# Kernel optimization log

Measured on AMD Instinct MI355X. Metric: run time of the kernel, lower is better.

The kernel has to match this reference:

```python
import jax, jax.numpy as jnp
import numpy as np

BONE_NUM = 16
THRESH = 0.7


def masked_l2(out, tar, mask):
    # out, tar: [B, C, H, W]; mask: [B, H, W]
    diff_norm = jnp.linalg.norm(out - tar, axis=1)          # [B, H, W]
    masked = jnp.where(mask > THRESH, diff_norm, 0.0)
    B = out.shape[0]
    flat_m = masked.reshape(B, -1)
    flat_d = diff_norm.reshape(B, -1)
    cnt = jnp.sum(flat_m != 0, axis=1)                       # device-side nonzero count
    per_sample = jnp.where(
        cnt > 0,
        flat_m.sum(axis=1) / jnp.maximum(cnt, 1).astype(flat_m.dtype),
        flat_d.mean(axis=1),
    )
    return per_sample.mean()


def pose_nocs_loss(pred_joint_map, pred_joint_score, out_mask, tar_joints):
    # pred_joint_map: [B, bn*3, H, W]; pred_joint_score: [B, bn, H, W]
    # out_mask: [B, H, W]; tar_joints: [B, bn, 3]
    B, _, H, W = pred_joint_map.shape
    bn = BONE_NUM
    jm = pred_joint_map.reshape(B, bn, 3, H, W) * out_mask[:, None, None]
    score = jax.nn.sigmoid(pred_joint_score) * out_mask[:, None]        # [B, bn, H, W]
    denom = score.reshape(B, bn, -1).sum(axis=2)[:, :, None, None] + 1e-5
    score_map = score / denom
    jm = jax.lax.stop_gradient(jm) * score_map[:, :, None]              # [B, bn, 3, H, W]
    pred_joint = jm.reshape(B, bn, 3, -1).sum(axis=3)                   # [B, bn, 3]
    loss = jnp.linalg.norm(pred_joint - tar_joints, axis=2).sum()
    return loss / (B * bn)


def setup_inputs() -> dict:
    key = jax.random.key(0)
    k1, k2, k3 = jax.random.split(key, 3)
    B, H, W = 4, 256, 256
    bn = BONE_NUM
    output = jax.random.normal(k1, (B, 4 + bn * 8 + 2, H, W), dtype=jnp.float32)
    tar_maps = jax.random.uniform(k2, (B, 4 + bn * 6 + 1, H, W), dtype=jnp.float32)
    tar_pose = jax.random.normal(k3, (B, bn, 6), dtype=jnp.float32)
    return {"output": output, "tar_maps": tar_maps, "tar_pose": tar_pose}


def reference(output, tar_maps, tar_pose):
    bn = BONE_NUM
    B = output.shape[0]

    # --- slice predictions ---
    pred_nocs = output[:, 0:3]
    mask_logits = output[:, 3]                                # sigmoid applied below
    pred_loc_map = jax.nn.sigmoid(output[:, 4:4 + bn * 3])
    pred_rot_map = jax.nn.sigmoid(output[:, 4 + bn * 3:4 + bn * 6])
    pred_skin_seg = output[:, 4 + bn * 6:4 + bn * 7 + 2]       # [B, bn+2, H, W]
    pred_joint_score = output[:, 4 + bn * 7 + 2:4 + bn * 8 + 2]  # [B, bn, H, W]

    # --- slice targets ---
    target_nocs = tar_maps[:, 0:3]
    target_mask = tar_maps[:, 3]
    tar_loc_map = jax.nn.sigmoid(tar_maps[:, 4:4 + bn * 3])
    tar_rot_map = jax.nn.sigmoid(tar_maps[:, 4 + bn * 3:4 + bn * 6])
    tar_skin_seg = tar_maps[:, 4 + bn * 6].astype(jnp.int32)   # [B, H, W]
    tar_loc = jax.nn.sigmoid(tar_pose[:, :, 0:3])
    tar_rot = jax.nn.sigmoid(tar_pose[:, :, 3:6])

    # --- BCE mask loss (on sigmoid(mask_logits) vs target_mask), stable form ---
    mask_loss = -jnp.mean(
        target_mask * jax.nn.log_sigmoid(mask_logits)
        + (1.0 - target_mask) * jax.nn.log_sigmoid(-mask_logits)
    )

    # --- masked L2 losses ---
    nocs_loss = masked_l2(pred_nocs, target_nocs, target_mask)
    loc_map_loss = masked_l2(pred_loc_map, tar_loc_map, target_mask)
    rot_map_loss = masked_l2(pred_rot_map, tar_rot_map, target_mask)

    # --- skinning cross entropy ---
    logits = jnp.transpose(pred_skin_seg, (0, 2, 3, 1)).reshape(-1, bn + 2)
    labels = tar_skin_seg.reshape(-1)
    logp = jax.nn.log_softmax(logits, axis=-1)
    skin_loss = -jnp.mean(jnp.take_along_axis(logp, labels[:, None], axis=1))

    # --- pose losses ---
    loc_loss = pose_nocs_loss(pred_loc_map, pred_joint_score, target_mask, tar_loc)
    rot_loss = pose_nocs_loss(pred_rot_map, pred_joint_score, target_mask, tar_rot)

    return jnp.stack([nocs_loss, mask_loss, loc_loss, loc_map_loss,
                      rot_loss, rot_map_loss, skin_loss])
```

## Files before the change

### kernel.cpp

```cpp
#include <hip/hip_runtime.h>
#include <math.h>

#define HW 65536
#define BN 16


__device__ __forceinline__ float fsig(float x) {
    return __builtin_amdgcn_rcpf(1.0f + __expf(-x));
}
__device__ __forceinline__ float sq(float x) { return x * x; }

__device__ __forceinline__ float wred(float v) {
#pragma unroll
    for (int off = 32; off; off >>= 1) v += __shfl_xor(v, off, 64);
    return v;
}

__global__ __launch_bounds__(256) void mvpm_pix2(const float* __restrict__ outp,
                                                 const float* __restrict__ tarp,
                                                 float* __restrict__ ws) {
    const int b = blockIdx.y;
    const int t = blockIdx.x * 256 + threadIdx.x;
    const int C2 = HW / 2;
    const float2* ob = (const float2*)(outp + (size_t)b * 134 * HW) + t;
    const float2* tb = (const float2*)(tarp + (size_t)b * 101 * HW) + t;
    const int lane = threadIdx.x & 63;
    const int wv = threadIdx.x >> 6;

    const float2 m2 = tb[3 * C2];
    const float2 ml = ob[3 * C2];
    const float2 a0 = ob[0], a1 = ob[C2], a2 = ob[2 * C2];
    const float2 b0 = tb[0], b1 = tb[C2], b2 = tb[2 * C2];

    const float bce =
        (m2.x * fminf(ml.x, 0.0f) + (1.0f - m2.x) * fminf(-ml.x, 0.0f)
         - __logf(1.0f + __expf(-fabsf(ml.x)))) +
        (m2.y * fminf(ml.y, 0.0f) + (1.0f - m2.y) * fminf(-ml.y, 0.0f)
         - __logf(1.0f + __expf(-fabsf(ml.y))));

    const float dnx = sqrtf(sq(a0.x - b0.x) + sq(a1.x - b1.x) + sq(a2.x - b2.x));
    const float dny = sqrtf(sq(a0.y - b0.y) + sq(a1.y - b1.y) + sq(a2.y - b2.y));
    const bool sx = m2.x > 0.7f, sy = m2.y > 0.7f;

    float2 x[18];
#pragma unroll
    for (int k = 0; k < 18; ++k) x[k] = ob[(100 + k) * C2];
    const float2 labf = tb[100 * C2];
    float mxx = x[0].x, mxy = x[0].y;
#pragma unroll
    for (int k = 1; k < 18; ++k) { mxx = fmaxf(mxx, x[k].x); mxy = fmaxf(mxy, x[k].y); }
    float sex = 0.0f, sey = 0.0f;
#pragma unroll
    for (int k = 0; k < 18; ++k) { sex += __expf(x[k].x - mxx); sey += __expf(x[k].y - mxy); }
    int labx = (int)labf.x; labx = labx < 0 ? 0 : (labx > 17 ? 17 : labx);
    int laby = (int)labf.y; laby = laby < 0 ? 0 : (laby > 17 ? 17 : laby);
    float xlx = x[0].x, xly = x[0].y;
#pragma unroll
    for (int k = 1; k < 18; ++k) { xlx = (labx == k) ? x[k].x : xlx;
                                   xly = (laby == k) ? x[k].y : xly; }
    const float skin = (mxx + __logf(sex) - xlx) + (mxy + __logf(sey) - xly);

    float dslx = 0.0f, dsly = 0.0f, dsrx = 0.0f, dsry = 0.0f;
#pragma unroll 2
    for (int j = 0; j < BN; ++j) {
        const int cl = (4 + 3 * j) * C2, cr = (52 + 3 * j) * C2;
        const float2 o0 = ob[cl], o1 = ob[cl + C2], o2 = ob[cl + 2 * C2];
        const float2 t0 = tb[cl], t1 = tb[cl + C2], t2 = tb[cl + 2 * C2];
        const float2 p0 = ob[cr], p1 = ob[cr + C2], p2 = ob[cr + 2 * C2];
        const float2 q0 = tb[cr], q1 = tb[cr + C2], q2 = tb[cr + 2 * C2];
        dslx += sq(fsig(o0.x) - fsig(t0.x)) + sq(fsig(o1.x) - fsig(t1.x))
              + sq(fsig(o2.x) - fsig(t2.x));
        dsly += sq(fsig(o0.y) - fsig(t0.y)) + sq(fsig(o1.y) - fsig(t1.y))
              + sq(fsig(o2.y) - fsig(t2.y));
        dsrx += sq(fsig(p0.x) - fsig(q0.x)) + sq(fsig(p1.x) - fsig(q1.x))
              + sq(fsig(p2.x) - fsig(q2.x));
        dsry += sq(fsig(p0.y) - fsig(q0.y)) + sq(fsig(p1.y) - fsig(q1.y))
              + sq(fsig(p2.y) - fsig(q2.y));
    }
    const float dnlx = sqrtf(dslx), dnly = sqrtf(dsly);
    const float dnrx = sqrtf(dsrx), dnry = sqrtf(dsry);

    float v[11];
    v[0]  = bce;
    v[1]  = skin;
    v[2]  = (sx ? dnx : 0.0f) + (sy ? dny : 0.0f);
    v[3]  = ((sx && dnx != 0.0f) ? 1.0f : 0.0f) + ((sy && dny != 0.0f) ? 1.0f : 0.0f);
    v[4]  = dnx + dny;
    v[5]  = (sx ? dnlx : 0.0f) + (sy ? dnly : 0.0f);
    v[6]  = ((sx && dnlx != 0.0f) ? 1.0f : 0.0f) + ((sy && dnly != 0.0f) ? 1.0f : 0.0f);
    v[7]  = dnlx + dnly;
    v[8]  = (sx ? dnrx : 0.0f) + (sy ? dnry : 0.0f);
    v[9]  = ((sx && dnrx != 0.0f) ? 1.0f : 0.0f) + ((sy && dnry != 0.0f) ? 1.0f : 0.0f);
    v[10] = dnrx + dnry;

#pragma unroll
    for (int off = 32; off; off >>= 1) {
#pragma unroll
        for (int i = 0; i < 11; ++i) v[i] += __shfl_xor(v[i], off, 64);
    }

    __shared__ float red[11][4];
    if (lane == 0) {
#pragma unroll
        for (int i = 0; i < 11; ++i) red[i][wv] = v[i];
    }
    __syncthreads();
    if (threadIdx.x < 11) {
        float s = red[threadIdx.x][0] + red[threadIdx.x][1] +
                  red[threadIdx.x][2] + red[threadIdx.x][3];
        int g = (threadIdx.x < 2) ? threadIdx.x : (2 + b * 9 + (threadIdx.x - 2));
        atomicAdd(&ws[g], s);
    }
}

__global__ __launch_bounds__(256) void mvpm_joint4(const float* __restrict__ outp,
                                                   const float* __restrict__ tarp,
                                                   float* __restrict__ ws) {
    const int bj = blockIdx.y;
    const int b = bj >> 4;
    const int j = bj & 15;
    const int C4 = HW / 4;
    const int idx = blockIdx.x * 256 + threadIdx.x;
    const float4* ob = (const float4*)(outp + (size_t)b * 134 * HW);
    const int lane = threadIdx.x & 63;
    const int wv = threadIdx.x >> 6;

    const float4 m  = ((const float4*)(tarp + (size_t)b * 101 * HW))[3 * C4 + idx];
    const float4 s  = ob[(118 + j) * C4 + idx];
    const float4 l0 = ob[(4 + 3 * j) * C4 + idx];
    const float4 l1 = ob[(5 + 3 * j) * C4 + idx];
    const float4 l2 = ob[(6 + 3 * j) * C4 + idx];
    const float4 r0 = ob[(52 + 3 * j) * C4 + idx];
    const float4 r1 = ob[(53 + 3 * j) * C4 + idx];
    const float4 r2 = ob[(54 + 3 * j) * C4 + idx];

    float wx = fsig(s.x) * m.x, wy = fsig(s.y) * m.y,
          wz = fsig(s.z) * m.z, ww = fsig(s.w) * m.w;
    float v[7];
    v[0] = wx + wy + wz + ww;
    wx *= m.x; wy *= m.y; wz *= m.z; ww *= m.w;
    v[1] = fsig(l0.x) * wx + fsig(l0.y) * wy + fsig(l0.z) * wz + fsig(l0.w) * ww;
    v[2] = fsig(l1.x) * wx + fsig(l1.y) * wy + fsig(l1.z) * wz + fsig(l1.w) * ww;
    v[3] = fsig(l2.x) * wx + fsig(l2.y) * wy + fsig(l2.z) * wz + fsig(l2.w) * ww;
    v[4] = fsig(r0.x) * wx + fsig(r0.y) * wy + fsig(r0.z) * wz + fsig(r0.w) * ww;
    v[5] = fsig(r1.x) * wx + fsig(r1.y) * wy + fsig(r1.z) * wz + fsig(r1.w) * ww;
    v[6] = fsig(r2.x) * wx + fsig(r2.y) * wy + fsig(r2.z) * wz + fsig(r2.w) * ww;

#pragma unroll
    for (int off = 32; off; off >>= 1) {
#pragma unroll
        for (int i = 0; i < 7; ++i) v[i] += __shfl_xor(v[i], off, 64);
    }

    __shared__ float red[7][4];
    if (lane == 0) {
#pragma unroll
        for (int i = 0; i < 7; ++i) red[i][wv] = v[i];
    }
    __syncthreads();
    if (threadIdx.x < 7) {
        float sum = red[threadIdx.x][0] + red[threadIdx.x][1] +
                    red[threadIdx.x][2] + red[threadIdx.x][3];
        atomicAdd(&ws[38 + bj * 7 + threadIdx.x], sum);
    }
}

__global__ __launch_bounds__(64) void mvpm_fin(const float* __restrict__ ws,
                                               const float* __restrict__ tp,
                                               float* __restrict__ o) {
    const int t = threadIdx.x;
    const int base = 38 + t * 7;

    float S = ws[base] + 1e-5f;
    float ln = 0.0f, rn = 0.0f;
#pragma unroll
    for (int c = 0; c < 3; ++c) {
        float pl = ws[base + 1 + c] / S;
        float tl = 1.0f / (1.0f + expf(-tp[t * 6 + c]));
        ln += (pl - tl) * (pl - tl);
        float pr = ws[base + 4 + c] / S;
        float tr = 1.0f / (1.0f + expf(-tp[t * 6 + 3 + c]));
        rn += (pr - tr) * (pr - tr);
    }
    ln = sqrtf(ln);
    rn = sqrtf(rn);
    float lsum = wred(ln);
    float rsum = wred(rn);

    if (t == 0) {
        float nocs = 0.0f, locm = 0.0f, rotm = 0.0f;
        for (int bb = 0; bb < 4; ++bb) {
            int ba = 2 + bb * 9;
            nocs += (ws[ba + 1] > 0.5f) ? ws[ba + 0] / ws[ba + 1] : ws[ba + 2] * (1.0f / HW);
            locm += (ws[ba + 4] > 0.5f) ? ws[ba + 3] / ws[ba + 4] : ws[ba + 5] * (1.0f / HW);
            rotm += (ws[ba + 7] > 0.5f) ? ws[ba + 6] / ws[ba + 7] : ws[ba + 8] * (1.0f / HW);
        }
        o[0] = nocs * 0.25f;
        o[1] = -ws[0] / (4.0f * HW);
        o[2] = lsum * (1.0f / 64.0f);
        o[3] = locm * 0.25f;
        o[4] = rsum * (1.0f / 64.0f);
        o[5] = rotm * 0.25f;
        o[6] = ws[1] / (4.0f * HW);
    }
}

extern "C" void kernel_launch(void* const* d_in, const int* in_sizes, int n_in,
                              void* d_out, int out_size, void* d_ws, size_t ws_size,
                              hipStream_t stream) {
    const float* outp = (const float*)d_in[0];
    const float* tarp = (const float*)d_in[1];
    const float* tpos = (const float*)d_in[2];
    float* o  = (float*)d_out;
    float* ws = (float*)d_ws;

    hipMemsetAsync(d_ws, 0, 486 * sizeof(float), stream);
    dim3 gA(HW / 512, 4);
    mvpm_pix2<<<gA, 256, 0, stream>>>(outp, tarp, ws);
    dim3 gB(HW / 1024, 64);
    mvpm_joint4<<<gB, 256, 0, stream>>>(outp, tarp, ws);
    mvpm_fin<<<1, 64, 0, stream>>>(ws, tpos, o);
}
```

Before: 291.8 us.

## Fuse per-pixel loss and joint-weighted sum kernels into one pass

Merges the pixel-loss kernel and the per-joint weighted-sum kernel into a single kernel, so the loc/rot map channels are read once and their sigmoids are reused for both the map L2 loss and the joint pose sums. It also moves from float2 to scalar per-thread loads with twice as many blocks. This removes a second full read of about 100 channels and one launch. The cost is 16 extra wave reductions per thread and more atomics per block, and narrower loads.

Measured after the change: 284.6 us. 2.5% less time.

```diff
diff --git a/kernel.cpp b/kernel.cpp
--- a/kernel.cpp
+++ b/kernel.cpp
@@ -16,152 +16,114 @@
     return v;
 }
 
-__global__ __launch_bounds__(256) void mvpm_pix2(const float* __restrict__ outp,
-                                                 const float* __restrict__ tarp,
-                                                 float* __restrict__ ws) {
+__global__ __launch_bounds__(256) void mvpm_fused(const float* __restrict__ outp,
+                                                  const float* __restrict__ tarp,
+                                                  float* __restrict__ ws) {
     const int b = blockIdx.y;
-    const int t = blockIdx.x * 256 + threadIdx.x;
-    const int C2 = HW / 2;
-    const float2* ob = (const float2*)(outp + (size_t)b * 134 * HW) + t;
-    const float2* tb = (const float2*)(tarp + (size_t)b * 101 * HW) + t;
+    const int p = blockIdx.x * 256 + threadIdx.x;
+    const float* ob = outp + (size_t)b * 134 * HW + p;
+    const float* tb = tarp + (size_t)b * 101 * HW + p;
     const int lane = threadIdx.x & 63;
     const int wv = threadIdx.x >> 6;
 
-    const float2 m2 = tb[3 * C2];
-    const float2 ml = ob[3 * C2];
-    const float2 a0 = ob[0], a1 = ob[C2], a2 = ob[2 * C2];
-    const float2 b0 = tb[0], b1 = tb[C2], b2 = tb[2 * C2];
+    __shared__ float jacc[BN][7][4];
+    __shared__ float red[11][4];
 
-    const float bce =
-        (m2.x * fminf(ml.x, 0.0f) + (1.0f - m2.x) * fminf(-ml.x, 0.0f)
-         - __logf(1.0f + __expf(-fabsf(ml.x)))) +
-        (m2.y * fminf(ml.y, 0.0f) + (1.0f - m2.y) * fminf(-ml.y, 0.0f)
-         - __logf(1.0f + __expf(-fabsf(ml.y))));
+    const float m  = tb[3 * HW];
+    const float ml = ob[3 * HW];
+    const float a0 = ob[0], a1 = ob[HW], a2 = ob[2 * HW];
+    const float b0 = tb[0], b1 = tb[HW], b2 = tb[2 * HW];
 
-    const float dnx = sqrtf(sq(a0.x - b0.x) + sq(a1.x - b1.x) + sq(a2.x - b2.x));
-    const float dny = sqrtf(sq(a0.y - b0.y) + sq(a1.y - b1.y) + sq(a2.y - b2.y));
-    const bool sx = m2.x > 0.7f, sy = m2.y > 0.7f;
+    const float bce = m * fminf(ml, 0.0f) + (1.0f - m) * fminf(-ml, 0.0f)
+                      - __logf(1.0f + __expf(-fabsf(ml)));
+    const float dn = sqrtf(sq(a0 - b0) + sq(a1 - b1) + sq(a2 - b2));
+    const bool sel = m > 0.7f;
+    const float mm = m * m;
 
-    float2 x[18];
+    float x[18];
 #pragma unroll
-    for (int k = 0; k < 18; ++k) x[k] = ob[(100 + k) * C2];
-    const float2 labf = tb[100 * C2];
-    float mxx = x[0].x, mxy = x[0].y;
+    for (int k = 0; k < 18; ++k) x[k] = ob[(100 + k) * HW];
+    const float labf = tb[100 * HW];
+    float mx = x[0];
 #pragma unroll
-    for (int k = 1; k < 18; ++k) { mxx = fmaxf(mxx, x[k].x); mxy = fmaxf(mxy, x[k].y); }
-    float sex = 0.0f, sey = 0.0f;
+    for (int k = 1; k < 18; ++k) mx = fmaxf(mx, x[k]);
+    float se = 0.0f;
 #pragma unroll
-    for (int k = 0; k < 18; ++k) { sex += __expf(x[k].x - mxx); sey += __expf(x[k].y - mxy); }
-    int labx = (int)labf.x; labx = labx < 0 ? 0 : (labx > 17 ? 17 : labx);
-    int laby = (int)labf.y; laby = laby < 0 ? 0 : (laby > 17 ? 17 : laby);
-    float xlx = x[0].x, xly = x[0].y;
+    for (int k = 0; k < 18; ++k) se += __expf(x[k] - mx);
+    int lab = (int)labf; lab = lab < 0 ? 0 : (lab > 17 ? 17 : lab);
+    float xl = x[0];
 #pragma unroll
-    for (int k = 1; k < 18; ++k) { xlx = (labx == k) ? x[k].x : xlx;
-                                   xly = (laby == k) ? x[k].y : xly; }
-    const float skin = (mxx + __logf(sex) - xlx) + (mxy + __logf(sey) - xly);
+    for (int k = 1; k < 18; ++k) xl = (lab == k) ? x[k] : xl;
+    const float skin = mx + __logf(se) - xl;
 
-    float dslx = 0.0f, dsly = 0.0f, dsrx = 0.0f, dsry = 0.0f;
+    float dsl = 0.0f, dsr = 0.0f;
 #pragma unroll 2
     for (int j = 0; j < BN; ++j) {
-        const int cl = (4 + 3 * j) * C2, cr = (52 + 3 * j) * C2;
-        const float2 o0 = ob[cl], o1 = ob[cl + C2], o2 = ob[cl + 2 * C2];
-        const float2 t0 = tb[cl], t1 = tb[cl + C2], t2 = tb[cl + 2 * C2];
-        const float2 p0 = ob[cr], p1 = ob[cr + C2], p2 = ob[cr + 2 * C2];
-        const float2 q0 = tb[cr], q1 = tb[cr + C2], q2 = tb[cr + 2 * C2];
-        dslx += sq(fsig(o0.x) - fsig(t0.x)) + sq(fsig(o1.x) - fsig(t1.x))
-              + sq(fsig(o2.x) - fsig(t2.x));
-        dsly += sq(fsig(o0.y) - fsig(t0.y)) + sq(fsig(o1.y) - fsig(t1.y))
-              + sq(fsig(o2.y) - fsig(t2.y));
-        dsrx += sq(fsig(p0.x) - fsig(q0.x)) + sq(fsig(p1.x) - fsig(q1.x))
-              + sq(fsig(p2.x) - fsig(q2.x));
-        dsry += sq(fsig(p0.y) - fsig(q0.y)) + sq(fsig(p1.y) - fsig(q1.y))
-              + sq(fsig(p2.y) - fsig(q2.y));
+        const int cl = (4 + 3 * j) * HW, cr = (52 + 3 * j) * HW;
+        const float o0 = ob[cl], o1 = ob[cl + HW], o2 = ob[cl + 2 * HW];
+        const float t0 = tb[cl], t1 = tb[cl + HW], t2 = tb[cl + 2 * HW];
+        const float p0 = ob[cr], p1 = ob[cr + HW], p2 = ob[cr + 2 * HW];
+        const float q0 = tb[cr], q1 = tb[cr + HW], q2 = tb[cr + 2 * HW];
+        const float sc = ob[(118 + j) * HW];
+
+        const float so0 = fsig(o0), so1 = fsig(o1), so2 = fsig(o2);
+        const float sp0 = fsig(p0), sp1 = fsig(p1), sp2 = fsig(p2);
+        dsl += sq(so0 - fsig(t0)) + sq(so1 - fsig(t1)) + sq(so2 - fsig(t2));
+        dsr += sq(sp0 - fsig(q0)) + sq(sp1 - fsig(q1)) + sq(sp2 - fsig(q2));
+
+        const float ss = fsig(sc);
+        const float w2 = ss * mm;
+        float u[7];
+        u[0] = ss * m;
+        u[1] = so0 * w2; u[2] = so1 * w2; u[3] = so2 * w2;
+        u[4] = sp0 * w2; u[5] = sp1 * w2; u[6] = sp2 * w2;
+
+#pragma unroll
+        for (int off = 32; off; off >>= 1) {
+#pragma unroll
+            for (int i = 0; i < 7; ++i) u[i] += __shfl_xor(u[i], off, 64);
+        }
+        if (lane == 0) {
+#pragma unroll
+            for (int i = 0; i < 7; ++i) jacc[j][i][wv] = u[i];
+        }
     }
-    const float dnlx = sqrtf(dslx), dnly = sqrtf(dsly);
-    const float dnrx = sqrtf(dsrx), dnry = sqrtf(dsry);
+    const float dnl = sqrtf(dsl), dnr = sqrtf(dsr);
 
     float v[11];
     v[0]  = bce;
     v[1]  = skin;
-    v[2]  = (sx ? dnx : 0.0f) + (sy ? dny : 0.0f);
-    v[3]  = ((sx && dnx != 0.0f) ? 1.0f : 0.0f) + ((sy && dny != 0.0f) ? 1.0f : 0.0f);
-    v[4]  = dnx + dny;
-    v[5]  = (sx ? dnlx : 0.0f) + (sy ? dnly : 0.0f);
-    v[6]  = ((sx && dnlx != 0.0f) ? 1.0f : 0.0f) + ((sy && dnly != 0.0f) ? 1.0f : 0.0f);
-    v[7]  = dnlx + dnly;
-    v[8]  = (sx ? dnrx : 0.0f) + (sy ? dnry : 0.0f);
-    v[9]  = ((sx && dnrx != 0.0f) ? 1.0f : 0.0f) + ((sy && dnry != 0.0f) ? 1.0f : 0.0f);
-    v[10] = dnrx + dnry;
+    v[2]  = sel ? dn : 0.0f;
+    v[3]  = (sel && dn != 0.0f) ? 1.0f : 0.0f;
+    v[4]  = dn;
+    v[5]  = sel ? dnl : 0.0f;
+    v[6]  = (sel && dnl != 0.0f) ? 1.0f : 0.0f;
+    v[7]  = dnl;
+    v[8]  = sel ? dnr : 0.0f;
+    v[9]  = (sel && dnr != 0.0f) ? 1.0f : 0.0f;
+    v[10] = dnr;
 
 #pragma unroll
     for (int off = 32; off; off >>= 1) {
 #pragma unroll
         for (int i = 0; i < 11; ++i) v[i] += __shfl_xor(v[i], off, 64);
     }
-
-    __shared__ float red[11][4];
     if (lane == 0) {
 #pragma unroll
         for (int i = 0; i < 11; ++i) red[i][wv] = v[i];
     }
     __syncthreads();
-    if (threadIdx.x < 11) {
-        float s = red[threadIdx.x][0] + red[threadIdx.x][1] +
-                  red[threadIdx.x][2] + red[threadIdx.x][3];
-        int g = (threadIdx.x < 2) ? threadIdx.x : (2 + b * 9 + (threadIdx.x - 2));
+
+    const int t = threadIdx.x;
+    if (t < 112) {
+        const int j = t / 7, c = t % 7;
+        const float s = jacc[j][c][0] + jacc[j][c][1] + jacc[j][c][2] + jacc[j][c][3];
+        atomicAdd(&ws[38 + (b * 16 + j) * 7 + c], s);
+    } else if (t >= 128 && t < 139) {
+        const int i = t - 128;
+        const float s = red[i][0] + red[i][1] + red[i][2] + red[i][3];
+        const int g = (i < 2) ? i : (2 + b * 9 + (i - 2));
         atomicAdd(&ws[g], s);
-    }
-}
-
-__global__ __launch_bounds__(256) void mvpm_joint4(const float* __restrict__ outp,
-                                                   const float* __restrict__ tarp,
-                                                   float* __restrict__ ws) {
-    const int bj = blockIdx.y;
-    const int b = bj >> 4;
-    const int j = bj & 15;
-    const int C4 = HW / 4;
-    const int idx = blockIdx.x * 256 + threadIdx.x;
-    const float4* ob = (const float4*)(outp + (size_t)b * 134 * HW);
-    const int lane = threadIdx.x & 63;
-    const int wv = threadIdx.x >> 6;
-
-    const float4 m  = ((const float4*)(tarp + (size_t)b * 101 * HW))[3 * C4 + idx];
-    const float4 s  = ob[(118 + j) * C4 + idx];
-    const float4 l0 = ob[(4 + 3 * j) * C4 + idx];
-    const float4 l1 = ob[(5 + 3 * j) * C4 + idx];
-    const float4 l2 = ob[(6 + 3 * j) * C4 + idx];
-    const float4 r0 = ob[(52 + 3 * j) * C4 + idx];
-    const float4 r1 = ob[(53 + 3 * j) * C4 + idx];
-    const float4 r2 = ob[(54 + 3 * j) * C4 + idx];
-
-    float wx = fsig(s.x) * m.x, wy = fsig(s.y) * m.y,
-          wz = fsig(s.z) * m.z, ww = fsig(s.w) * m.w;
-    float v[7];
-    v[0] = wx + wy + wz + ww;
-    wx *= m.x; wy *= m.y; wz *= m.z; ww *= m.w;
-    v[1] = fsig(l0.x) * wx + fsig(l0.y) * wy + fsig(l0.z) * wz + fsig(l0.w) * ww;
-    v[2] = fsig(l1.x) * wx + fsig(l1.y) * wy + fsig(l1.z) * wz + fsig(l1.w) * ww;
-    v[3] = fsig(l2.x) * wx + fsig(l2.y) * wy + fsig(l2.z) * wz + fsig(l2.w) * ww;
-    v[4] = fsig(r0.x) * wx + fsig(r0.y) * wy + fsig(r0.z) * wz + fsig(r0.w) * ww;
-    v[5] = fsig(r1.x) * wx + fsig(r1.y) * wy + fsig(r1.z) * wz + fsig(r1.w) * ww;
-    v[6] = fsig(r2.x) * wx + fsig(r2.y) * wy + fsig(r2.z) * wz + fsig(r2.w) * ww;
-
-#pragma unroll
-    for (int off = 32; off; off >>= 1) {
-#pragma unroll
-        for (int i = 0; i < 7; ++i) v[i] += __shfl_xor(v[i], off, 64);
-    }
-
-    __shared__ float red[7][4];
-    if (lane == 0) {
-#pragma unroll
-        for (int i = 0; i < 7; ++i) red[i][wv] = v[i];
-    }
-    __syncthreads();
-    if (threadIdx.x < 7) {
-        float sum = red[threadIdx.x][0] + red[threadIdx.x][1] +
-                    red[threadIdx.x][2] + red[threadIdx.x][3];
-        atomicAdd(&ws[38 + bj * 7 + threadIdx.x], sum);
     }
 }
 
@@ -215,9 +177,7 @@
     float* ws = (float*)d_ws;
 
     hipMemsetAsync(d_ws, 0, 486 * sizeof(float), stream);
-    dim3 gA(HW / 512, 4);
-    mvpm_pix2<<<gA, 256, 0, stream>>>(outp, tarp, ws);
-    dim3 gB(HW / 1024, 64);
-    mvpm_joint4<<<gB, 256, 0, stream>>>(outp, tarp, ws);
+    dim3 g(HW / 256, 4);
+    mvpm_fused<<<g, 256, 0, stream>>>(outp, tarp, ws);
     mvpm_fin<<<1, 64, 0, stream>>>(ws, tpos, o);
 }
```

## Fuse joint-weighted reduction into per-pixel kernel with double-buffered channel loads

Applied to the files above, without the earlier changes.

Merges the separate joint reduction kernel into the per-pixel loss kernel, so the loc/rot map channels are read once and their sigmoids are shared between the masked L2 and the score-weighted joint sums. Score channels are loaded in the same pass. The per-bone loop is software-pipelined with two register buffers, and the 7 joint sums are reduced with a split shuffle scheme: 8-lane partial reductions select one value per lane, followed by a cross-group reduction into shared memory. This removes one kernel launch and a second full read of about 112 channels, at the cost of higher register pressure, which may lower occupancy.

Result: slower. 379.4 us (+30.0%).

```diff
diff --git a/kernel.cpp b/kernel.cpp
--- a/kernel.cpp
+++ b/kernel.cpp
@@ -16,16 +16,20 @@
     return v;
 }
 
-__global__ __launch_bounds__(256) void mvpm_pix2(const float* __restrict__ outp,
-                                                 const float* __restrict__ tarp,
-                                                 float* __restrict__ ws) {
+__global__ __launch_bounds__(256) void mvpm_fused(const float* __restrict__ outp,
+                                                  const float* __restrict__ tarp,
+                                                  float* __restrict__ ws) {
     const int b = blockIdx.y;
-    const int t = blockIdx.x * 256 + threadIdx.x;
+    const int t2 = blockIdx.x * 256 + threadIdx.x;
     const int C2 = HW / 2;
-    const float2* ob = (const float2*)(outp + (size_t)b * 134 * HW) + t;
-    const float2* tb = (const float2*)(tarp + (size_t)b * 101 * HW) + t;
+    const float2* ob = (const float2*)(outp + (size_t)b * 134 * HW) + t2;
+    const float2* tb = (const float2*)(tarp + (size_t)b * 101 * HW) + t2;
     const int lane = threadIdx.x & 63;
     const int wv = threadIdx.x >> 6;
+    const int l7 = lane & 7;
+
+    __shared__ float jacc[BN][7][4];
+    __shared__ float red[11][4];
 
     const float2 m2 = tb[3 * C2];
     const float2 ml = ob[3 * C2];
@@ -41,6 +45,7 @@
     const float dnx = sqrtf(sq(a0.x - b0.x) + sq(a1.x - b1.x) + sq(a2.x - b2.x));
     const float dny = sqrtf(sq(a0.y - b0.y) + sq(a1.y - b1.y) + sq(a2.y - b2.y));
     const bool sx = m2.x > 0.7f, sy = m2.y > 0.7f;
+    const float mmx = m2.x * m2.x, mmy = m2.y * m2.y;
 
     float2 x[18];
 #pragma unroll
@@ -61,22 +66,80 @@
     const float skin = (mxx + __logf(sex) - xlx) + (mxy + __logf(sey) - xly);
 
     float dslx = 0.0f, dsly = 0.0f, dsrx = 0.0f, dsry = 0.0f;
-#pragma unroll 2
+    float rj[BN];
+
+#define LOADJ(buf, j)                                                          \
+    {                                                                          \
+        const int cl = (4 + 3 * (j)) * C2, cr = (52 + 3 * (j)) * C2;           \
+        buf[0] = ob[cl]; buf[1] = ob[cl + C2]; buf[2] = ob[cl + 2 * C2];       \
+        buf[3] = tb[cl]; buf[4] = tb[cl + C2]; buf[5] = tb[cl + 2 * C2];       \
+        buf[6] = ob[cr]; buf[7] = ob[cr + C2]; buf[8] = ob[cr + 2 * C2];       \
+        buf[9] = tb[cr]; buf[10] = tb[cr + C2]; buf[11] = tb[cr + 2 * C2];     \
+        buf[12] = ob[(118 + (j)) * C2];                                        \
+    }
+
+#define COMPUTEJ(buf, j)                                                       \
+    {                                                                          \
+        const float so0x = fsig(buf[0].x), so0y = fsig(buf[0].y);              \
+        const float so1x = fsig(buf[1].x), so1y = fsig(buf[1].y);              \
+        const float so2x = fsig(buf[2].x), so2y = fsig(buf[2].y);              \
+        const float sp0x = fsig(buf[6].x), sp0y = fsig(buf[6].y);              \
+        const float sp1x = fsig(buf[7].x), sp1y = fsig(buf[7].y);              \
+        const float sp2x = fsig(buf[8].x), sp2y = fsig(buf[8].y);              \
+        dslx += sq(so0x - fsig(buf[3].x)) + sq(so1x - fsig(buf[4].x))          \
+              + sq(so2x - fsig(buf[5].x));                                     \
+        dsly += sq(so0y - fsig(buf[3].y)) + sq(so1y - fsig(buf[4].y))          \
+              + sq(so2y - fsig(buf[5].y));                                     \
+        dsrx += sq(sp0x - fsig(buf[9].x)) + sq(sp1x - fsig(buf[10].x))         \
+              + sq(sp2x - fsig(buf[11].x));                                    \
+        dsry += sq(sp0y - fsig(buf[9].y)) + sq(sp1y - fsig(buf[10].y))         \
+              + sq(sp2y - fsig(buf[11].y));                                    \
+        const float ssx = fsig(buf[12].x), ssy = fsig(buf[12].y);              \
+        const float wx = ssx * mmx, wy = ssy * mmy;                            \
+        float u[7];                                                            \
+        u[0] = ssx * m2.x + ssy * m2.y;                                        \
+        u[1] = so0x * wx + so0y * wy;                                          \
+        u[2] = so1x * wx + so1y * wy;                                          \
+        u[3] = so2x * wx + so2y * wy;                                          \
+        u[4] = sp0x * wx + sp0y * wy;                                          \
+        u[5] = sp1x * wx + sp1y * wy;                                          \
+        u[6] = sp2x * wx + sp2y * wy;                                          \
+        _Pragma("unroll")                                                      \
+        for (int off = 1; off <= 4; off <<= 1) {                               \
+            _Pragma("unroll")                                                  \
+            for (int i = 0; i < 7; ++i) u[i] += __shfl_xor(u[i], off, 64);     \
+        }                                                                      \
+        float r = u[0];                                                        \
+        r = (l7 == 1) ? u[1] : r;                                              \
+        r = (l7 == 2) ? u[2] : r;                                              \
+        r = (l7 == 3) ? u[3] : r;                                              \
+        r = (l7 == 4) ? u[4] : r;                                              \
+        r = (l7 == 5) ? u[5] : r;                                              \
+        r = (l7 == 6) ? u[6] : r;                                              \
+        rj[j] = r;                                                             \
+    }
+
+    float2 A[13], B[13];
+    LOADJ(A, 0);
+#pragma unroll
+    for (int jj = 0; jj < BN; jj += 2) {
+        LOADJ(B, jj + 1);
+        COMPUTEJ(A, jj);
+        if (jj + 2 < BN) LOADJ(A, jj + 2);
+        COMPUTEJ(B, jj + 1);
+    }
+#undef LOADJ
+#undef COMPUTEJ
+
+#pragma unroll
     for (int j = 0; j < BN; ++j) {
-        const int cl = (4 + 3 * j) * C2, cr = (52 + 3 * j) * C2;
-        const float2 o0 = ob[cl], o1 = ob[cl + C2], o2 = ob[cl + 2 * C2];
-        const float2 t0 = tb[cl], t1 = tb[cl + C2], t2 = tb[cl + 2 * C2];
-        const float2 p0 = ob[cr], p1 = ob[cr + C2], p2 = ob[cr + 2 * C2];
-        const float2 q0 = tb[cr], q1 = tb[cr + C2], q2 = tb[cr + 2 * C2];
-        dslx += sq(fsig(o0.x) - fsig(t0.x)) + sq(fsig(o1.x) - fsig(t1.x))
-              + sq(fsig(o2.x) - fsig(t2.x));
-        dsly += sq(fsig(o0.y) - fsig(t0.y)) + sq(fsig(o1.y) - fsig(t1.y))
-              + sq(fsig(o2.y) - fsig(t2.y));
-        dsrx += sq(fsig(p0.x) - fsig(q0.x)) + sq(fsig(p1.x) - fsig(q1.x))
-              + sq(fsig(p2.x) - fsig(q2.x));
-        dsry += sq(fsig(p0.y) - fsig(q0.y)) + sq(fsig(p1.y) - fsig(q1.y))
-              + sq(fsig(p2.y) - fsig(q2.y));
-    }
+        float r = rj[j];
+        r += __shfl_xor(r, 8, 64);
+        r += __shfl_xor(r, 16, 64);
+        r += __shfl_xor(r, 32, 64);
+        if (lane < 7) jacc[j][lane][wv] = r;
+    }
+
     const float dnlx = sqrtf(dslx), dnly = sqrtf(dsly);
     const float dnrx = sqrtf(dsrx), dnry = sqrtf(dsry);
 
@@ -98,70 +161,22 @@
 #pragma unroll
         for (int i = 0; i < 11; ++i) v[i] += __shfl_xor(v[i], off, 64);
     }
-
-    __shared__ float red[11][4];
     if (lane == 0) {
 #pragma unroll
         for (int i = 0; i < 11; ++i) red[i][wv] = v[i];
     }
     __syncthreads();
-    if (threadIdx.x < 11) {
-        float s = red[threadIdx.x][0] + red[threadIdx.x][1] +
-                  red[threadIdx.x][2] + red[threadIdx.x][3];
-        int g = (threadIdx.x < 2) ? threadIdx.x : (2 + b * 9 + (threadIdx.x - 2));
+
+    const int t = threadIdx.x;
+    if (t < 112) {
+        const int j = t / 7, c = t % 7;
+        const float s = jacc[j][c][0] + jacc[j][c][1] + jacc[j][c][2] + jacc[j][c][3];
+        atomicAdd(&ws[38 + (b * 16 + j) * 7 + c], s);
+    } else if (t >= 128 && t < 139) {
+        const int i = t - 128;
+        const float s = red[i][0] + red[i][1] + red[i][2] + red[i][3];
+        const int g = (i < 2) ? i : (2 + b * 9 + (i - 2));
         atomicAdd(&ws[g], s);
-    }
-}
-
-__global__ __launch_bounds__(256) void mvpm_joint4(const float* __restrict__ outp,
-                                                   const float* __restrict__ tarp,
-                                                   float* __restrict__ ws) {
-    const int bj = blockIdx.y;
-    const int b = bj >> 4;
-    const int j = bj & 15;
-    const int C4 = HW / 4;
-    const int idx = blockIdx.x * 256 + threadIdx.x;
-    const float4* ob = (const float4*)(outp + (size_t)b * 134 * HW);
-    const int lane = threadIdx.x & 63;
-    const int wv = threadIdx.x >> 6;
-
-    const float4 m  = ((const float4*)(tarp + (size_t)b * 101 * HW))[3 * C4 + idx];
-    const float4 s  = ob[(118 + j) * C4 + idx];
-    const float4 l0 = ob[(4 + 3 * j) * C4 + idx];
-    const float4 l1 = ob[(5 + 3 * j) * C4 + idx];
-    const float4 l2 = ob[(6 + 3 * j) * C4 + idx];
-    const float4 r0 = ob[(52 + 3 * j) * C4 + idx];
-    const float4 r1 = ob[(53 + 3 * j) * C4 + idx];
-    const float4 r2 = ob[(54 + 3 * j) * C4 + idx];
-
-    float wx = fsig(s.x) * m.x, wy = fsig(s.y) * m.y,
-          wz = fsig(s.z) * m.z, ww = fsig(s.w) * m.w;
-    float v[7];
-    v[0] = wx + wy + wz + ww;
-    wx *= m.x; wy *= m.y; wz *= m.z; ww *= m.w;
-    v[1] = fsig(l0.x) * wx + fsig(l0.y) * wy + fsig(l0.z) * wz + fsig(l0.w) * ww;
-    v[2] = fsig(l1.x) * wx + fsig(l1.y) * wy + fsig(l1.z) * wz + fsig(l1.w) * ww;
-    v[3] = fsig(l2.x) * wx + fsig(l2.y) * wy + fsig(l2.z) * wz + fsig(l2.w) * ww;
-    v[4] = fsig(r0.x) * wx + fsig(r0.y) * wy + fsig(r0.z) * wz + fsig(r0.w) * ww;
-    v[5] = fsig(r1.x) * wx + fsig(r1.y) * wy + fsig(r1.z) * wz + fsig(r1.w) * ww;
-    v[6] = fsig(r2.x) * wx + fsig(r2.y) * wy + fsig(r2.z) * wz + fsig(r2.w) * ww;
-
-#pragma unroll
-    for (int off = 32; off; off >>= 1) {
-#pragma unroll
-        for (int i = 0; i < 7; ++i) v[i] += __shfl_xor(v[i], off, 64);
-    }
-
-    __shared__ float red[7][4];
-    if (lane == 0) {
-#pragma unroll
-        for (int i = 0; i < 7; ++i) red[i][wv] = v[i];
-    }
-    __syncthreads();
-    if (threadIdx.x < 7) {
-        float sum = red[threadIdx.x][0] + red[threadIdx.x][1] +
-                    red[threadIdx.x][2] + red[threadIdx.x][3];
-        atomicAdd(&ws[38 + bj * 7 + threadIdx.x], sum);
     }
 }
 
@@ -215,9 +230,7 @@
     float* ws = (float*)d_ws;
 
     hipMemsetAsync(d_ws, 0, 486 * sizeof(float), stream);
-    dim3 gA(HW / 512, 4);
-    mvpm_pix2<<<gA, 256, 0, stream>>>(outp, tarp, ws);
-    dim3 gB(HW / 1024, 64);
-    mvpm_joint4<<<gB, 256, 0, stream>>>(outp, tarp, ws);
+    dim3 g(HW / 512, 4);
+    mvpm_fused<<<g, 256, 0, stream>>>(outp, tarp, ws);
     mvpm_fin<<<1, 64, 0, stream>>>(ws, tpos, o);
 }
```
